# Optimization experiments

Hardware: AMD Instinct MI355X
Metric: run time of the kernel (lower is better)

The kernel has to match this reference:

```python
import jax, jax.numpy as jnp
import numpy as np
import math

D_MODEL, N_HEADS, D_FF = 1024, 16, 4096
D_K = D_MODEL // N_HEADS
B, S = 4, 2048
EPS = 1e-5


def layer_norm(x, gamma, beta):
    mean = jnp.mean(x, axis=-1, keepdims=True)
    var = jnp.mean((x - mean) ** 2, axis=-1, keepdims=True)  # unbiased=False
    return gamma * (x - mean) / jnp.sqrt(var + EPS) + beta


def setup_inputs() -> dict:
    key = jax.random.key(0)
    ks = jax.random.split(key, 7)
    std_attn = math.sqrt(2.0 / (D_MODEL + D_MODEL))
    std_ff1 = math.sqrt(2.0 / (D_MODEL + D_FF))
    std_ff2 = math.sqrt(2.0 / (D_FF + D_MODEL))
    return {
        "x": jax.random.normal(ks[0], (B, S, D_MODEL), jnp.float32),
        "W_q": jax.random.normal(ks[1], (D_MODEL, D_MODEL), jnp.float32) * std_attn,
        "W_k": jax.random.normal(ks[2], (D_MODEL, D_MODEL), jnp.float32) * std_attn,
        "W_v": jax.random.normal(ks[3], (D_MODEL, D_MODEL), jnp.float32) * std_attn,
        "W_o": jax.random.normal(ks[4], (D_MODEL, D_MODEL), jnp.float32) * std_attn,
        "W1": jax.random.normal(ks[5], (D_MODEL, D_FF), jnp.float32) * std_ff1,
        "b1": jnp.zeros((D_FF,), jnp.float32),
        "W2": jax.random.normal(ks[6], (D_FF, D_MODEL), jnp.float32) * std_ff2,
        "b2": jnp.zeros((D_MODEL,), jnp.float32),
        "ln1_gamma": jnp.ones((D_MODEL,), jnp.float32),
        "ln1_beta": jnp.zeros((D_MODEL,), jnp.float32),
        "ln2_gamma": jnp.ones((D_MODEL,), jnp.float32),
        "ln2_beta": jnp.zeros((D_MODEL,), jnp.float32),
    }


def reference(x, W_q, W_k, W_v, W_o, W1, b1, W2, b2,
              ln1_gamma, ln1_beta, ln2_gamma, ln2_beta):
    b, s, d = x.shape
    # pre-LN attention block
    ln1 = layer_norm(x, ln1_gamma, ln1_beta)
    q = (ln1 @ W_q).reshape(b, s, N_HEADS, D_K)
    k = (ln1 @ W_k).reshape(b, s, N_HEADS, D_K)
    v = (ln1 @ W_v).reshape(b, s, N_HEADS, D_K)
    scores = jnp.einsum("bqhd,bkhd->bhqk", q, k) / math.sqrt(D_K)
    attn = jax.nn.softmax(scores, axis=-1)
    ctx = jnp.einsum("bhqk,bkhd->bqhd", attn, v).reshape(b, s, d)
    attn_out = ctx @ W_o
    attn_residual = x + attn_out
    # pre-LN FFN block
    ln2 = layer_norm(attn_residual, ln2_gamma, ln2_beta)
    ff = jax.nn.relu(ln2 @ W1 + b1) @ W2 + b2
    return attn_residual + ff
```

## Files before the change

kernel.cpp:

```cpp
#include <hip/hip_runtime.h>
#include <hip/hip_bf16.h>

typedef __attribute__((ext_vector_type(4))) float  floatx4;
typedef __attribute__((ext_vector_type(8))) short  shortx8;
typedef __attribute__((ext_vector_type(4))) short  shortx4;

__device__ __forceinline__ short f2bf(float f) {
    unsigned u = __float_as_uint(f);
    u += 0x7fffu + ((u >> 16) & 1u);
    return (short)(u >> 16);
}
__device__ __forceinline__ float bf2f(short s) {
    return __uint_as_float(((unsigned)(unsigned short)s) << 16);
}
__device__ __forceinline__ float fast_exp2(float x) {
#if __has_builtin(__builtin_amdgcn_exp2f)
    return __builtin_amdgcn_exp2f(x);
#else
    return exp2f(x);
#endif
}

__device__ __forceinline__ void load_lds16(const void* g, void* l) {
    __builtin_amdgcn_global_load_lds(
        (const __attribute__((address_space(1))) unsigned int*)g,
        (__attribute__((address_space(3))) unsigned int*)l,
        16, 0, 0);
}

__global__ __launch_bounds__(256)
void transpose_w(const float* __restrict__ src, short* __restrict__ dst, int K, int N)
{
    __shared__ __align__(16) float tile[32][33];
    const int n0 = blockIdx.x * 32, k0 = blockIdx.y * 32;
    const int tx = threadIdx.x & 31, ty = threadIdx.x >> 5;
    for (int i = 0; i < 32; i += 8)
        tile[ty + i][tx] = src[(size_t)(k0 + ty + i) * N + n0 + tx];
    __syncthreads();
    for (int i = 0; i < 32; i += 8)
        dst[(size_t)(n0 + ty + i) * K + k0 + tx] = f2bf(tile[tx][ty + i]);
}

__global__ __launch_bounds__(256)
void ln_bf16(const float* __restrict__ x, const float* __restrict__ g,
             const float* __restrict__ be, short* __restrict__ out)
{
    const int row = blockIdx.x;
    const int tid = threadIdx.x;
    const float4 v = reinterpret_cast<const float4*>(x + (size_t)row * 1024)[tid];
    float s  = v.x + v.y + v.z + v.w;
    float ss = v.x * v.x + v.y * v.y + v.z * v.z + v.w * v.w;
    for (int off = 32; off > 0; off >>= 1) {
        s  += __shfl_down(s,  off);
        ss += __shfl_down(ss, off);
    }
    __shared__ float rs[4], rss[4];
    const int wave = tid >> 6, lane = tid & 63;
    if (lane == 0) { rs[wave] = s; rss[wave] = ss; }
    __syncthreads();
    const float S    = rs[0] + rs[1] + rs[2] + rs[3];
    const float SS   = rss[0] + rss[1] + rss[2] + rss[3];
    const float mean = S * (1.0f / 1024.0f);
    const float var  = SS * (1.0f / 1024.0f) - mean * mean;
    const float rstd = rsqrtf(var + 1e-5f);
    const float4 gg = reinterpret_cast<const float4*>(g)[tid];
    const float4 bb = reinterpret_cast<const float4*>(be)[tid];
    shortx4 o;
    o[0] = f2bf(gg.x * ((v.x - mean) * rstd) + bb.x);
    o[1] = f2bf(gg.y * ((v.y - mean) * rstd) + bb.y);
    o[2] = f2bf(gg.z * ((v.z - mean) * rstd) + bb.z);
    o[3] = f2bf(gg.w * ((v.w - mean) * rstd) + bb.w);
    *reinterpret_cast<shortx4*>(out + (size_t)row * 1024 + tid * 4) = o;
}

template <int EPI>
__global__ __launch_bounds__(256)
void gemm_bt(const short* __restrict__ A, const short* __restrict__ Bt,
             short* __restrict__ Cb, float* __restrict__ Cf,
             const float* __restrict__ bias, const float* __restrict__ resid,
             int M, int N, int K)
{
    __shared__ __align__(16) short As[128 * 32];
    __shared__ __align__(16) short Bs[128 * 32];
    const int tid  = threadIdx.x;
    const int wave = tid >> 6;
    const int lane = tid & 63;
    const int quad = lane >> 4;
    const int l16  = lane & 15;
    const int wm = wave >> 1, wn = wave & 1;
    const size_t bm = (size_t)blockIdx.y * 128;
    const size_t bn = (size_t)blockIdx.x * 128;

    floatx4 acc[4][4];
    for (int i = 0; i < 4; i++)
        for (int j = 0; j < 4; j++)
            acc[i][j] = (floatx4){0.f, 0.f, 0.f, 0.f};

    const int c0 = wave * 2, c1 = wave * 2 + 1;
    const int rA0 = c0 * 16 + (lane >> 2);
    const int rA1 = c1 * 16 + (lane >> 2);
    const int colOff = (lane & 3) * 8;

    for (int k0 = 0; k0 < K; k0 += 32) {
        load_lds16(A  + (bm + rA0) * (size_t)K + k0 + colOff, &As[c0 * 512]);
        load_lds16(A  + (bm + rA1) * (size_t)K + k0 + colOff, &As[c1 * 512]);
        load_lds16(Bt + (bn + rA0) * (size_t)K + k0 + colOff, &Bs[c0 * 512]);
        load_lds16(Bt + (bn + rA1) * (size_t)K + k0 + colOff, &Bs[c1 * 512]);
        __syncthreads();
        shortx8 af[4], bf[4];
        for (int mi = 0; mi < 4; mi++)
            af[mi] = *(const shortx8*)&As[(wm * 64 + mi * 16 + l16) * 32 + quad * 8];
        for (int ni = 0; ni < 4; ni++)
            bf[ni] = *(const shortx8*)&Bs[(wn * 64 + ni * 16 + l16) * 32 + quad * 8];
        for (int mi = 0; mi < 4; mi++)
            for (int ni = 0; ni < 4; ni++)
                acc[mi][ni] = __builtin_amdgcn_mfma_f32_16x16x32_bf16(
                    af[mi], bf[ni], acc[mi][ni], 0, 0, 0);
        __syncthreads();
    }

    for (int mi = 0; mi < 4; mi++) {
        for (int ni = 0; ni < 4; ni++) {
            const size_t row0 = bm + wm * 64 + mi * 16 + quad * 4;
            const size_t col  = bn + wn * 64 + ni * 16 + l16;
            for (int r = 0; r < 4; r++) {
                float v = acc[mi][ni][r];
                const size_t idx = (row0 + r) * (size_t)N + col;
                if (EPI == 0) {
                    Cb[idx] = f2bf(v);
                } else if (EPI == 1) {
                    v += bias[col];
                    Cb[idx] = f2bf(v > 0.f ? v : 0.f);
                } else if (EPI == 2) {
                    Cf[idx] = resid[idx] + v;
                } else {
                    v += bias[col];
                    Cf[idx] = resid[idx] + v;
                }
            }
        }
    }
}

__global__ __launch_bounds__(256)
void transpose_v(const short* __restrict__ qkv, short* __restrict__ vt)
{
    __shared__ __align__(16) short tile[64][65];
    const int st = blockIdx.x, h = blockIdx.y, b = blockIdx.z;
    const int t = threadIdx.x;
    for (int i = 0; i < 2; i++) {
        const int idx = i * 256 + t;
        const int s = idx >> 3, dg = idx & 7;
        shortx8 val = *(const shortx8*)&qkv[(size_t)(b * 2048 + st * 64 + s) * 3072
                                           + 2048 + h * 64 + dg * 8];
        for (int u = 0; u < 8; u++) tile[s][dg * 8 + u] = val[u];
    }
    __syncthreads();
    const int d = t >> 2, sg = (t & 3) * 16;
    shortx8 lo, hi;
    for (int i = 0; i < 8; i++) {
        lo[i] = tile[sg + i][d];
        hi[i] = tile[sg + 8 + i][d];
    }
    const size_t base = ((size_t)(b * 16 + h) * 64 + d) * 2048 + st * 64 + sg;
    *(shortx8*)&vt[base]     = lo;
    *(shortx8*)&vt[base + 8] = hi;
}

__global__ __launch_bounds__(512)
void attention_kernel(const short* __restrict__ qkv, const short* __restrict__ vt,
                      short* __restrict__ ctx)
{
    const int qt = blockIdx.x, h = blockIdx.y, b = blockIdx.z;
    const int tid  = threadIdx.x;
    const int wave = tid >> 6;
    const int lane = tid & 63;
    const int quad = lane >> 4;
    const int l16  = lane & 15;

    __shared__ __align__(16) short Ks[64 * 72];
    __shared__ __align__(16) short Vs[64 * 72];
    __shared__ __align__(16) short Ps[8][16 * 72];

    const int q0 = qt * 128 + wave * 16;
    const float qscale = 0.125f * 1.44269504088896f;
    const short* qrow = qkv + (size_t)(b * 2048 + q0 + l16) * 3072 + h * 64;
    shortx8 qf[2];
    for (int kk = 0; kk < 2; kk++) {
        shortx8 raw = *(const shortx8*)&qrow[kk * 32 + quad * 8];
        for (int j = 0; j < 8; j++) raw[j] = f2bf(bf2f(raw[j]) * qscale);
        qf[kk] = raw;
    }

    shortx8 vones;
    for (int j = 0; j < 8; j++) vones[j] = (short)0x3F80;

    floatx4 accO[5];
    for (int dt = 0; dt < 5; dt++) accO[dt] = (floatx4){0.f, 0.f, 0.f, 0.f};

    const short* kbase = qkv + (size_t)(b * 2048) * 3072 + 1024 + h * 64;
    const short* vbase = vt + ((size_t)(b * 16 + h) * 64) * 2048;
    short* const psw = &Ps[wave][0];

    const int ss = tid >> 3, sdg = tid & 7;

    for (int kt = 0; kt < 32; ++kt) {
        __syncthreads();
        {
            shortx8 kv = *(const shortx8*)&kbase[(size_t)(kt * 64 + ss) * 3072 + sdg * 8];
            *(shortx8*)&Ks[ss * 72 + sdg * 8] = kv;
            shortx8 vv = *(const shortx8*)&vbase[(size_t)ss * 2048 + kt * 64 + sdg * 8];
            *(shortx8*)&Vs[ss * 72 + sdg * 8] = vv;
        }
        __syncthreads();

        floatx4 st[4];
        for (int nt = 0; nt < 4; nt++) {
            shortx8 kf0 = *(const shortx8*)&Ks[(nt * 16 + l16) * 72 + 0 * 32 + quad * 8];
            shortx8 kf1 = *(const shortx8*)&Ks[(nt * 16 + l16) * 72 + 1 * 32 + quad * 8];
            floatx4 c = (floatx4){0.f, 0.f, 0.f, 0.f};
            c = __builtin_amdgcn_mfma_f32_16x16x32_bf16(kf0, qf[0], c, 0, 0, 0);
            c = __builtin_amdgcn_mfma_f32_16x16x32_bf16(kf1, qf[1], c, 0, 0, 0);
            st[nt] = c;
        }

        for (int nt = 0; nt < 4; nt++) {
            float2 p01, p23;
            p01.x = fast_exp2(st[nt][0]);
            p01.y = fast_exp2(st[nt][1]);
            p23.x = fast_exp2(st[nt][2]);
            p23.y = fast_exp2(st[nt][3]);
            union { __hip_bfloat162 h2[2]; uint2 u; } pk;
            pk.h2[0] = __float22bfloat162_rn(p01);
            pk.h2[1] = __float22bfloat162_rn(p23);
            *(uint2*)&psw[l16 * 72 + nt * 16 + quad * 4] = pk.u;
        }
        asm volatile("s_waitcnt lgkmcnt(0)" ::: "memory");

        shortx8 pf0 = *(const shortx8*)&psw[l16 * 72 + 0 * 32 + quad * 8];
        shortx8 pf1 = *(const shortx8*)&psw[l16 * 72 + 1 * 32 + quad * 8];

        for (int dt = 0; dt < 4; dt++) {
            shortx8 vf0 = *(const shortx8*)&Vs[(dt * 16 + l16) * 72 + 0 * 32 + quad * 8];
            shortx8 vf1 = *(const shortx8*)&Vs[(dt * 16 + l16) * 72 + 1 * 32 + quad * 8];
            floatx4 c = accO[dt];
            c = __builtin_amdgcn_mfma_f32_16x16x32_bf16(pf0, vf0, c, 0, 0, 0);
            c = __builtin_amdgcn_mfma_f32_16x16x32_bf16(pf1, vf1, c, 0, 0, 0);
            accO[dt] = c;
        }
        {
            floatx4 c = accO[4];
            c = __builtin_amdgcn_mfma_f32_16x16x32_bf16(pf0, vones, c, 0, 0, 0);
            c = __builtin_amdgcn_mfma_f32_16x16x32_bf16(pf1, vones, c, 0, 0, 0);
            accO[4] = c;
        }
    }

    const int qg = q0 + quad * 4;
    for (int r = 0; r < 4; r++) {
        const float inv = 1.0f / accO[4][r];
        for (int dt = 0; dt < 4; dt++)
            ctx[(size_t)(b * 2048 + qg + r) * 1024 + h * 64 + dt * 16 + l16]
                = f2bf(accO[dt][r] * inv);
    }
}

extern "C" void kernel_launch(void* const* d_in, const int* in_sizes, int n_in,
                              void* d_out, int out_size, void* d_ws, size_t ws_size,
                              hipStream_t stream)
{
    const float* x   = (const float*)d_in[0];
    const float* Wq  = (const float*)d_in[1];
    const float* Wk  = (const float*)d_in[2];
    const float* Wv  = (const float*)d_in[3];
    const float* Wo  = (const float*)d_in[4];
    const float* W1  = (const float*)d_in[5];
    const float* b1  = (const float*)d_in[6];
    const float* W2  = (const float*)d_in[7];
    const float* b2  = (const float*)d_in[8];
    const float* g1  = (const float*)d_in[9];
    const float* be1 = (const float*)d_in[10];
    const float* g2  = (const float*)d_in[11];
    const float* be2 = (const float*)d_in[12];
    float* out = (float*)d_out;
    char*  ws  = (char*)d_ws;

    const size_t MiB = 1u << 20;
    short* regA   = (short*)(ws);
    short* qkv    = (short*)(ws + 16 * MiB);
    short* vt     = (short*)(ws + 64 * MiB);
    short* ff1    = qkv;
    short* Wqkv_t = (short*)(ws + 80 * MiB);
    short* Wo_t   = (short*)(ws + 86 * MiB);
    short* W1_t   = (short*)(ws + 88 * MiB);
    short* W2_t   = (short*)(ws + 96 * MiB);

    const dim3 blk(256);

    transpose_w<<<dim3(32, 32),  blk, 0, stream>>>(Wq, Wqkv_t,                  1024, 1024);
    transpose_w<<<dim3(32, 32),  blk, 0, stream>>>(Wk, Wqkv_t + 1024 * 1024,    1024, 1024);
    transpose_w<<<dim3(32, 32),  blk, 0, stream>>>(Wv, Wqkv_t + 2 * 1024 * 1024,1024, 1024);
    transpose_w<<<dim3(32, 32),  blk, 0, stream>>>(Wo, Wo_t,                    1024, 1024);
    transpose_w<<<dim3(128, 32), blk, 0, stream>>>(W1, W1_t,                    1024, 4096);
    transpose_w<<<dim3(32, 128), blk, 0, stream>>>(W2, W2_t,                    4096, 1024);

    ln_bf16<<<8192, blk, 0, stream>>>(x, g1, be1, regA);
    gemm_bt<0><<<dim3(24, 64), blk, 0, stream>>>(regA, Wqkv_t, qkv, nullptr, nullptr, nullptr,
                                                 8192, 3072, 1024);
    transpose_v<<<dim3(32, 16, 4), blk, 0, stream>>>(qkv, vt);
    attention_kernel<<<dim3(16, 16, 4), dim3(512), 0, stream>>>(qkv, vt, regA);
    gemm_bt<2><<<dim3(8, 64), blk, 0, stream>>>(regA, Wo_t, nullptr, out, nullptr, x,
                                                8192, 1024, 1024);
    ln_bf16<<<8192, blk, 0, stream>>>(out, g2, be2, regA);
    gemm_bt<1><<<dim3(32, 64), blk, 0, stream>>>(regA, W1_t, ff1, nullptr, b1, nullptr,
                                                 8192, 4096, 1024);
    gemm_bt<3><<<dim3(8, 64), blk, 0, stream>>>(ff1, W2_t, nullptr, out, b2, out,
                                                8192, 1024, 4096);
}
```

Measured before the change: 585.8 us.

## Use 32x32 MFMA tiles in attention with 256-query blocks and scalar row sums

The attention kernel switches from 16x16x32 to 32x32x16 bf16 MFMA, so each wave handles 32 query rows and each block 256 queries, which halves the grid. K/V tiles loaded into LDS are reused across twice as many queries, cutting global loads and barriers per query. The softmax denominator is now accumulated in registers from the exp values rather than through an extra MFMA against a ones vector. The cost is higher register pressure from two 16-float accumulators, and with 512 blocks there may be fewer waves to spread across the CUs.

New measurement: 572.6 us. -2.3%, faster.

```diff
diff --git a/kernel.cpp b/kernel.cpp
--- a/kernel.cpp
+++ b/kernel.cpp
@@ -1,9 +1,10 @@
 #include <hip/hip_runtime.h>
 #include <hip/hip_bf16.h>
 
-typedef __attribute__((ext_vector_type(4))) float  floatx4;
-typedef __attribute__((ext_vector_type(8))) short  shortx8;
-typedef __attribute__((ext_vector_type(4))) short  shortx4;
+typedef __attribute__((ext_vector_type(4)))  float  floatx4;
+typedef __attribute__((ext_vector_type(16))) float  floatx16;
+typedef __attribute__((ext_vector_type(8)))  short  shortx8;
+typedef __attribute__((ext_vector_type(4)))  short  shortx4;
 
 __device__ __forceinline__ short f2bf(float f) {
     unsigned u = __float_as_uint(f);
@@ -167,7 +168,7 @@
     *(shortx8*)&vt[base + 8] = hi;
 }
 
-__global__ __launch_bounds__(512)
+__global__ __launch_bounds__(512, 4)
 void attention_kernel(const short* __restrict__ qkv, const short* __restrict__ vt,
                       short* __restrict__ ctx)
 {
@@ -175,32 +176,32 @@
     const int tid  = threadIdx.x;
     const int wave = tid >> 6;
     const int lane = tid & 63;
-    const int quad = lane >> 4;
-    const int l16  = lane & 15;
+    const int l32  = lane & 31;
+    const int hf   = lane >> 5;
 
     __shared__ __align__(16) short Ks[64 * 72];
     __shared__ __align__(16) short Vs[64 * 72];
-    __shared__ __align__(16) short Ps[8][16 * 72];
-
-    const int q0 = qt * 128 + wave * 16;
+    __shared__ __align__(16) short Ps[8][32 * 72];
+
+    const int q0 = qt * 256 + wave * 32;
     const float qscale = 0.125f * 1.44269504088896f;
-    const short* qrow = qkv + (size_t)(b * 2048 + q0 + l16) * 3072 + h * 64;
-    shortx8 qf[2];
-    for (int kk = 0; kk < 2; kk++) {
-        shortx8 raw = *(const shortx8*)&qrow[kk * 32 + quad * 8];
+    const short* qrow = qkv + (size_t)(b * 2048 + q0 + l32) * 3072 + h * 64;
+    shortx8 qf[4];
+    for (int dk = 0; dk < 4; dk++) {
+        shortx8 raw = *(const shortx8*)&qrow[dk * 16 + hf * 8];
         for (int j = 0; j < 8; j++) raw[j] = f2bf(bf2f(raw[j]) * qscale);
-        qf[kk] = raw;
-    }
-
-    shortx8 vones;
-    for (int j = 0; j < 8; j++) vones[j] = (short)0x3F80;
-
-    floatx4 accO[5];
-    for (int dt = 0; dt < 5; dt++) accO[dt] = (floatx4){0.f, 0.f, 0.f, 0.f};
+        qf[dk] = raw;
+    }
+
+    floatx16 accO[2];
+    for (int t = 0; t < 2; t++)
+        for (int r = 0; r < 16; r++) accO[t][r] = 0.f;
+    float lsum = 0.f;
 
     const short* kbase = qkv + (size_t)(b * 2048) * 3072 + 1024 + h * 64;
     const short* vbase = vt + ((size_t)(b * 16 + h) * 64) * 2048;
     short* const psw = &Ps[wave][0];
+    unsigned* const pswd = (unsigned*)psw;
 
     const int ss = tid >> 3, sdg = tid & 7;
 
@@ -214,55 +215,57 @@
         }
         __syncthreads();
 
-        floatx4 st[4];
-        for (int nt = 0; nt < 4; nt++) {
-            shortx8 kf0 = *(const shortx8*)&Ks[(nt * 16 + l16) * 72 + 0 * 32 + quad * 8];
-            shortx8 kf1 = *(const shortx8*)&Ks[(nt * 16 + l16) * 72 + 1 * 32 + quad * 8];
-            floatx4 c = (floatx4){0.f, 0.f, 0.f, 0.f};
-            c = __builtin_amdgcn_mfma_f32_16x16x32_bf16(kf0, qf[0], c, 0, 0, 0);
-            c = __builtin_amdgcn_mfma_f32_16x16x32_bf16(kf1, qf[1], c, 0, 0, 0);
-            st[nt] = c;
-        }
-
-        for (int nt = 0; nt < 4; nt++) {
-            float2 p01, p23;
-            p01.x = fast_exp2(st[nt][0]);
-            p01.y = fast_exp2(st[nt][1]);
-            p23.x = fast_exp2(st[nt][2]);
-            p23.y = fast_exp2(st[nt][3]);
+        for (int t = 0; t < 2; t++) {
+            floatx16 c;
+            for (int r = 0; r < 16; r++) c[r] = 0.f;
+            for (int dk = 0; dk < 4; dk++) {
+                shortx8 kf = *(const shortx8*)&Ks[(t * 32 + l32) * 72 + dk * 16 + hf * 8];
+                c = __builtin_amdgcn_mfma_f32_32x32x16_bf16(kf, qf[dk], c, 0, 0, 0);
+            }
+            for (int R = 0; R < 4; R++) {
+                float2 a, bb;
+                a.x  = fast_exp2(c[4 * R + 0]);
+                a.y  = fast_exp2(c[4 * R + 1]);
+                bb.x = fast_exp2(c[4 * R + 2]);
+                bb.y = fast_exp2(c[4 * R + 3]);
+                lsum += (a.x + a.y) + (bb.x + bb.y);
+                union { __hip_bfloat162 h2[2]; uint2 u; } pk;
+                pk.h2[0] = __float22bfloat162_rn(a);
+                pk.h2[1] = __float22bfloat162_rn(bb);
+                *(uint2*)&pswd[l32 * 36 + t * 16 + 4 * R + 2 * hf] = pk.u;
+            }
+        }
+        asm volatile("s_waitcnt lgkmcnt(0)" ::: "memory");
+
+        shortx8 pf[4];
+        for (int sk = 0; sk < 4; sk++)
+            pf[sk] = *(const shortx8*)&psw[l32 * 72 + sk * 16 + hf * 8];
+
+        for (int t = 0; t < 2; t++) {
+            floatx16 c = accO[t];
+            for (int sk = 0; sk < 4; sk++) {
+                shortx8 vf = *(const shortx8*)&Vs[(t * 32 + l32) * 72 + sk * 16 + hf * 8];
+                c = __builtin_amdgcn_mfma_f32_32x32x16_bf16(vf, pf[sk], c, 0, 0, 0);
+            }
+            accO[t] = c;
+        }
+    }
+
+    const float lfull = lsum + __shfl_xor(lsum, 32);
+    const float inv = 1.0f / lfull;
+    const size_t crow = (size_t)(b * 2048 + q0 + l32) * 1024 + h * 64;
+    for (int t = 0; t < 2; t++)
+        for (int R = 0; R < 4; R++) {
+            float2 a, bb;
+            a.x  = accO[t][4 * R + 0] * inv;
+            a.y  = accO[t][4 * R + 1] * inv;
+            bb.x = accO[t][4 * R + 2] * inv;
+            bb.y = accO[t][4 * R + 3] * inv;
             union { __hip_bfloat162 h2[2]; uint2 u; } pk;
-            pk.h2[0] = __float22bfloat162_rn(p01);
-            pk.h2[1] = __float22bfloat162_rn(p23);
-            *(uint2*)&psw[l16 * 72 + nt * 16 + quad * 4] = pk.u;
-        }
-        asm volatile("s_waitcnt lgkmcnt(0)" ::: "memory");
-
-        shortx8 pf0 = *(const shortx8*)&psw[l16 * 72 + 0 * 32 + quad * 8];
-        shortx8 pf1 = *(const shortx8*)&psw[l16 * 72 + 1 * 32 + quad * 8];
-
-        for (int dt = 0; dt < 4; dt++) {
-            shortx8 vf0 = *(const shortx8*)&Vs[(dt * 16 + l16) * 72 + 0 * 32 + quad * 8];
-            shortx8 vf1 = *(const shortx8*)&Vs[(dt * 16 + l16) * 72 + 1 * 32 + quad * 8];
-            floatx4 c = accO[dt];
-            c = __builtin_amdgcn_mfma_f32_16x16x32_bf16(pf0, vf0, c, 0, 0, 0);
-            c = __builtin_amdgcn_mfma_f32_16x16x32_bf16(pf1, vf1, c, 0, 0, 0);
-            accO[dt] = c;
-        }
-        {
-            floatx4 c = accO[4];
-            c = __builtin_amdgcn_mfma_f32_16x16x32_bf16(pf0, vones, c, 0, 0, 0);
-            c = __builtin_amdgcn_mfma_f32_16x16x32_bf16(pf1, vones, c, 0, 0, 0);
-            accO[4] = c;
-        }
-    }
-
-    const int qg = q0 + quad * 4;
-    for (int r = 0; r < 4; r++) {
-        const float inv = 1.0f / accO[4][r];
-        for (int dt = 0; dt < 4; dt++)
-            ctx[(size_t)(b * 2048 + qg + r) * 1024 + h * 64 + dt * 16 + l16]
-                = f2bf(accO[dt][r] * inv);
-    }
+            pk.h2[0] = __float22bfloat162_rn(a);
+            pk.h2[1] = __float22bfloat162_rn(bb);
+            *(uint2*)&ctx[crow + t * 32 + 8 * R + 4 * hf] = pk.u;
+        }
 }
 
 extern "C" void kernel_launch(void* const* d_in, const int* in_sizes, int n_in,
@@ -308,7 +311,7 @@
     gemm_bt<0><<<dim3(24, 64), blk, 0, stream>>>(regA, Wqkv_t, qkv, nullptr, nullptr, nullptr,
                                                  8192, 3072, 1024);
     transpose_v<<<dim3(32, 16, 4), blk, 0, stream>>>(qkv, vt);
-    attention_kernel<<<dim3(16, 16, 4), dim3(512), 0, stream>>>(qkv, vt, regA);
+    attention_kernel<<<dim3(8, 16, 4), dim3(512), 0, stream>>>(qkv, vt, regA);
     gemm_bt<2><<<dim3(8, 64), blk, 0, stream>>>(regA, Wo_t, nullptr, out, nullptr, x,
                                                 8192, 1024, 1024);
     ln_bf16<<<8192, blk, 0, stream>>>(out, g2, be2, regA);
```
